# Kernel tuning notes

Measured on AMD Instinct MI355X. Metric: run time of the kernel, lower is better.

Reference implementation:

```python
import jax, jax.numpy as jnp
import numpy as np

NTS = ["User", "Group", "Computer", "Resource", "AIAgent"]
NCNT = [60000, 20000, 40000, 40000, 10000]
FEAT = [22, 6, 14, 5, 9]
# (src_nt_idx, dst_nt_idx) for the 7 active relations:
# User-MemberOf->Group, Group-MemberOf->Group, User-AdminTo->Computer,
# User-ActuallyAccessed->Resource, Computer-LSASSAccessible->Computer,
# AIAgent-AgentCanAccess->Resource, User-GenericAll->User
REL = [(0, 1), (1, 1), (0, 2), (0, 3), (2, 2), (4, 3), (0, 0)]
H, NH, L = 128, 4, 3
HD = H // NH
R = len(REL)
E = 40000


def _forward(xs, Wins, b_in, Wq, Wk, Wv, Wmsg, bmsg, rel_imp, Wo, bo, ln_g, ln_b,
             Wr1, br1, Wr2, br2, We1, be1, We2, be2, edge_index, edge_weight, theta):
    elu = jax.nn.elu
    # input projections + ELU
    h = [elu(x @ W + b_in[i]) for i, (x, W) in enumerate(zip(xs, Wins))]
    # differentiable control suppression: higher theta -> lower edge weight
    ew = edge_weight * (1.0 - jax.nn.sigmoid(theta))[:, None]  # [R, E]
    scale = HD ** -0.5
    for l in range(L):
        agg = [[] for _ in NTS]
        imps = [[] for _ in NTS]
        for r, (si, di) in enumerate(REL):
            src, dst = edge_index[r, 0], edge_index[r, 1]
            nd = h[di].shape[0]
            q = (h[di][dst] @ Wq[l, r]).reshape(-1, NH, HD)
            k = (h[si][src] @ Wk[l, r]).reshape(-1, NH, HD)
            v = (h[si][src] @ Wv[l, r]).reshape(-1, NH, HD)
            s = (q * k).sum(-1) * scale * ew[r][:, None]          # [E, NH]
            m = jax.ops.segment_max(s, dst, num_segments=nd)       # per-dst max
            ex = jnp.exp(s - m[dst])
            z = jax.ops.segment_sum(ex, dst, num_segments=nd)
            p = ex / (z[dst] + 1e-10)                              # neighborhood softmax
            msg = (v * p[..., None]).reshape(-1, H) @ Wmsg[l, r] + bmsg[l, r]
            rw = jax.nn.sigmoid(rel_imp[l, r])
            agg[di].append(jax.ops.segment_sum(msg * rw, dst, num_segments=nd))
            imps[di].append(rw)
        nh = []
        for i in range(len(NTS)):
            if agg[i]:
                w = jax.nn.softmax(jax.lax.stop_gradient(jnp.stack(imps[i])))
                comb = jnp.einsum('r,rnh->nh', w, jnp.stack(agg[i]))
                y = h[i] + comb @ Wo[l, i] + bo[l, i]
                mu = y.mean(-1, keepdims=True)
                var = ((y - mu) ** 2).mean(-1, keepdims=True)
                nh.append((y - mu) / jnp.sqrt(var + 1e-5) * ln_g[l, i] + ln_b[l, i])
            else:
                nh.append(h[i])
        h = [elu(y) for y in nh]
    risks = tuple(jax.nn.sigmoid(elu(hi @ Wr1 + br1) @ Wr2 + br2) for hi in h)
    eps = []
    for r, (si, di) in enumerate(REL):
        comb = jnp.concatenate([h[si][edge_index[r, 0]], h[di][edge_index[r, 1]]], -1)
        eps.append(jax.nn.sigmoid(elu(comb @ We1 + be1) @ We2 + be2))
    return risks + tuple(eps)


def setup_inputs() -> dict:
    key = jax.random.key(0)
    ks = iter(jax.random.split(key, 64))
    d = {}
    for nt, n, f in zip(NTS, NCNT, FEAT):
        d["x_" + nt] = jax.random.normal(next(ks), (n, f), jnp.float32)
    ei = []
    for si, di in REL:
        src = jax.random.randint(next(ks), (E,), 0, NCNT[si])
        dst = jax.random.randint(next(ks), (E,), 0, NCNT[di])
        ei.append(jnp.stack([src, dst]))
    d["edge_index"] = jnp.stack(ei).astype(jnp.int32)
    d["edge_weight"] = jax.random.uniform(next(ks), (R, E), jnp.float32)
    d["theta"] = jax.random.normal(next(ks), (R,), jnp.float32)

    def lin(k, i, o):
        return jax.random.normal(k, (i, o), jnp.float32) / float(np.sqrt(i))

    for nt, f in zip(NTS, FEAT):
        d["Win_" + nt] = lin(next(ks), f, H)
    d["b_in"] = jnp.zeros((len(NTS), H), jnp.float32)
    for nm in ["Wq", "Wk", "Wv", "Wmsg"]:
        d[nm] = jax.random.normal(next(ks), (L, R, H, H), jnp.float32) / float(np.sqrt(H))
    d["bmsg"] = jnp.zeros((L, R, H), jnp.float32)
    d["rel_imp"] = jnp.ones((L, R), jnp.float32)
    d["Wo"] = jax.random.normal(next(ks), (L, len(NTS), H, H), jnp.float32) / float(np.sqrt(H))
    d["bo"] = jnp.zeros((L, len(NTS), H), jnp.float32)
    d["ln_g"] = jnp.ones((L, len(NTS), H), jnp.float32)
    d["ln_b"] = jnp.zeros((L, len(NTS), H), jnp.float32)
    d["Wr1"] = lin(next(ks), H, H // 2)
    d["br1"] = jnp.zeros((H // 2,), jnp.float32)
    d["Wr2"] = lin(next(ks), H // 2, 1)
    d["br2"] = jnp.zeros((1,), jnp.float32)
    d["We1"] = lin(next(ks), 2 * H, H)
    d["be1"] = jnp.zeros((H,), jnp.float32)
    d["We2"] = lin(next(ks), H, 1)
    d["be2"] = jnp.zeros((1,), jnp.float32)
    return d


def reference(x_User, x_Group, x_Computer, x_Resource, x_AIAgent,
              edge_index, edge_weight, theta,
              Win_User, Win_Group, Win_Computer, Win_Resource, Win_AIAgent, b_in,
              Wq, Wk, Wv, Wmsg, bmsg, rel_imp, Wo, bo, ln_g, ln_b,
              Wr1, br1, Wr2, br2, We1, be1, We2, be2):
    xs = [x_User, x_Group, x_Computer, x_Resource, x_AIAgent]
    Wins = [Win_User, Win_Group, Win_Computer, Win_Resource, Win_AIAgent]
    return _forward(xs, Wins, b_in, Wq, Wk, Wv, Wmsg, bmsg, rel_imp, Wo, bo,
                    ln_g, ln_b, Wr1, br1, Wr2, br2, We1, be1, We2, be2,
                    edge_index, edge_weight, theta)
```

## Files before the change

### kernel.cpp

```cpp
#include <hip/hip_runtime.h>

#define CDIV(a,b) (((a)+(b)-1)/(b))
#define EE 40000
#define TOTROWS 170000
#define NDOFF 60001
#define NCHK 59
#define G_PCAT 2657

typedef unsigned short ushort_t;
typedef short bf16x8 __attribute__((ext_vector_type(8)));
typedef float f32x4 __attribute__((ext_vector_type(4)));

__device__ __forceinline__ float eluf(float x) { return x > 0.f ? x : expf(x) - 1.f; }
__device__ __forceinline__ float sigf(float x) { return 1.f / (1.f + expf(-x)); }
__device__ __forceinline__ float b2f(ushort_t u) { return __uint_as_float(((unsigned)u) << 16); }
__device__ __forceinline__ ushort_t f2b(float f) {
  unsigned x = __float_as_uint(f);
  x += 0x7FFFu + ((x >> 16) & 1u);
  return (ushort_t)(x >> 16);
}
__device__ __forceinline__ unsigned pk2(float lo, float hi) {
  return (unsigned)f2b(lo) | ((unsigned)f2b(hi) << 16);
}
__device__ __forceinline__ float2 b2f2(unsigned u) {
  return make_float2(__uint_as_float(u << 16), __uint_as_float(u & 0xFFFF0000u));
}

__constant__ const int NDD_C[7] = {20000, 20000, 40000, 40000, 40000, 40000, 60000};

__device__ __forceinline__ void stage_B128(char* Bs, int tid, const ushort_t* Bt) {
#pragma unroll
  for (int i = 0; i < 8; i++) {
    int u = tid + i * 256;
    int nrow = u >> 4;
    uint4 w = *(const uint4*)(Bt + (size_t)u * 8);
    *(uint4*)(Bs + ((u * 16) ^ ((nrow & 7) << 4))) = w;
  }
}

__device__ __forceinline__ void stage_A_bf16(char* As, int tid, const ushort_t* Ab, int base, int n) {
#pragma unroll
  for (int i = 0; i < 4; i++) {
    int u = tid + i * 256;
    int row = u >> 4;
    int grow = base + row;
    uint4 v = make_uint4(0, 0, 0, 0);
    if (grow < n) v = *(const uint4*)&Ab[(size_t)grow * 128 + (u & 15) * 8];
    *(uint4*)(As + ((u * 16) ^ ((row & 7) << 4))) = v;
  }
}

template<int NF>
__device__ __forceinline__ void mfma_core(const char* As, const char* Bs, int lane, int wcol,
                                          f32x4 (&acc)[4][NF]) {
  int i16 = lane & 15, seg = lane >> 4;
#pragma unroll
  for (int s = 0; s < 4; s++) {
    bf16x8 a[4], b[NF];
#pragma unroll
    for (int m = 0; m < 4; m++) {
      int row = m * 16 + i16;
      a[m] = *(const bf16x8*)(As + ((row * 256 + s * 64 + seg * 16) ^ ((row & 7) << 4)));
    }
#pragma unroll
    for (int nn = 0; nn < NF; nn++) {
      int nr = wcol + nn * 16 + i16;
      b[nn] = *(const bf16x8*)(Bs + ((nr * 256 + s * 64 + seg * 16) ^ ((nr & 7) << 4)));
    }
#pragma unroll
    for (int m = 0; m < 4; m++)
#pragma unroll
      for (int nn = 0; nn < NF; nn++)
        acc[m][nn] = __builtin_amdgcn_mfma_f32_16x16x32_bf16(a[m], b[nn], acc[m][nn], 0, 0, 0);
  }
}

__global__ void prep_scalars(const float* __restrict__ theta, const float* __restrict__ rel_imp,
                             float* __restrict__ scal) {
  int t = threadIdx.x;
  if (t < 7) scal[t] = 1.f - sigf(theta[t]);
  if (t < 21) {
    const int partner[7] = {1, 0, 4, 5, 2, 3, -1};
    int l = t / 7, r = t % 7;
    float rw = sigf(rel_imp[t]);
    float w;
    if (partner[r] < 0) w = 1.f;
    else {
      float rwp = sigf(rel_imp[l * 7 + partner[r]]);
      float e0 = expf(rw), e1 = expf(rwp);
      w = e0 / (e0 + e1);
    }
    scal[8 + t] = w * rw;
  }
}

__global__ __launch_bounds__(256) void transpose_weights(
    const float* __restrict__ Wq, const float* __restrict__ Wk, const float* __restrict__ Wv,
    const float* __restrict__ Wmsg, const float* __restrict__ Wo, const float* __restrict__ We1,
    ushort_t* __restrict__ Wt) {
  int mat = blockIdx.x;
  const float* src;
  if (mat < 21)      src = Wq   + (size_t)mat * 16384;
  else if (mat < 42) src = Wk   + (size_t)(mat - 21) * 16384;
  else if (mat < 63) src = Wv   + (size_t)(mat - 42) * 16384;
  else if (mat < 84) src = Wmsg + (size_t)(mat - 63) * 16384;
  else if (mat < 99) src = Wo   + (size_t)(mat - 84) * 16384;
  else               src = We1  + (size_t)(mat - 99) * 16384;
  __shared__ ushort_t lds[16384];
  int t = threadIdx.x;
  for (int i = 0; i < 64; i++) {
    int u = t + i * 256;
    int k = u >> 7;
    int byte = (u * 2) ^ ((k & 15) << 2);
    *(ushort_t*)((char*)lds + byte) = f2b(src[u]);
  }
  __syncthreads();
  ushort_t* dst = Wt + (size_t)mat * 16384;
  for (int i = 0; i < 64; i++) {
    int u = t + i * 256;
    int n = u >> 7, k = u & 127;
    int byte = ((k * 128 + n) * 2) ^ ((k & 15) << 2);
    dst[u] = *(ushort_t*)((char*)lds + byte);
  }
}

__global__ void transpose_wr1(const float* __restrict__ Wr1, ushort_t* __restrict__ Wt101) {
  int u = blockIdx.x * 256 + threadIdx.x;
  int n = u >> 7, k = u & 127;
  Wt101[u] = f2b(Wr1[k * 64 + n]);
}

template<int F>
__device__ __forceinline__ void inproj_compute(const float* xs, const float* Ws, const float* b2,
                                               ushort_t* hptr, int base, int n, int tid) {
  int cp = tid & 63, rg = tid >> 6;
  float wc0[F], wc1[F];
#pragma unroll
  for (int f = 0; f < F; f++) {
    wc0[f] = Ws[f * 128 + cp * 2];
    wc1[f] = Ws[f * 128 + cp * 2 + 1];
  }
  float bb0 = b2[cp * 2], bb1 = b2[cp * 2 + 1];
  for (int i = 0; i < 16; i++) {
    int row = rg * 16 + i, grow = base + row;
    if (grow >= n) break;
    float a0 = bb0, a1 = bb1;
#pragma unroll
    for (int f = 0; f < F; f++) {
      float xv = xs[row * F + f];
      a0 = fmaf(xv, wc0[f], a0);
      a1 = fmaf(xv, wc1[f], a1);
    }
    *(unsigned*)&hptr[(size_t)grow * 128 + cp * 2] = pk2(eluf(a0), eluf(a1));
  }
}

__global__ __launch_bounds__(256) void in_proj_all(
    const float* __restrict__ x0, const float* __restrict__ x1, const float* __restrict__ x2,
    const float* __restrict__ x3, const float* __restrict__ x4,
    const float* __restrict__ W0, const float* __restrict__ W1, const float* __restrict__ W2,
    const float* __restrict__ W3, const float* __restrict__ W4,
    const float* __restrict__ b_in, ushort_t* __restrict__ h) {
  __shared__ float xs[64 * 22];
  __shared__ float Ws[22 * 128];
  int bb = blockIdx.x, tid = threadIdx.x;
  int ti, lb;
  if (bb < 938)       { ti = 0; lb = bb; }
  else if (bb < 1251) { ti = 1; lb = bb - 938; }
  else if (bb < 1876) { ti = 2; lb = bb - 1251; }
  else if (bb < 2501) { ti = 3; lb = bb - 1876; }
  else                { ti = 4; lb = bb - 2501; }
  const int ROFF_[5] = {0, 60000, 80000, 120000, 160000};
  const int NCNT_[5] = {60000, 20000, 40000, 40000, 10000};
  const int FEAT_[5] = {22, 6, 14, 5, 9};
  const float* xp = (ti == 0) ? x0 : (ti == 1) ? x1 : (ti == 2) ? x2 : (ti == 3) ? x3 : x4;
  const float* Wp = (ti == 0) ? W0 : (ti == 1) ? W1 : (ti == 2) ? W2 : (ti == 3) ? W3 : W4;
  int F = FEAT_[ti], n = NCNT_[ti], base = lb * 64;
  for (int u = tid; u < F * 128; u += 256) Ws[u] = Wp[u];
  for (int u = tid; u < 64 * F; u += 256) {
    int row = u / F, f = u - row * F, grow = base + row;
    xs[u] = (grow < n) ? xp[(size_t)grow * F + f] : 0.f;
  }
  __syncthreads();
  ushort_t* hptr = h + (size_t)ROFF_[ti] * 128;
  const float* b2 = b_in + ti * 128;
  switch (ti) {
    case 0: inproj_compute<22>(xs, Ws, b2, hptr, base, n, tid); break;
    case 1: inproj_compute<6>(xs, Ws, b2, hptr, base, n, tid); break;
    case 2: inproj_compute<14>(xs, Ws, b2, hptr, base, n, tid); break;
    case 3: inproj_compute<5>(xs, Ws, b2, hptr, base, n, tid); break;
    default: inproj_compute<9>(xs, Ws, b2, hptr, base, n, tid); break;
  }
}

__global__ void csr_clear(int* __restrict__ counts) {
  int idx = blockIdx.x * 256 + threadIdx.x;
  if (idx < 7 * NDOFF) counts[idx] = 0;
}

__global__ void csr_hist(const int* __restrict__ ei, int* __restrict__ counts) {
  int idx = blockIdx.x * 256 + threadIdx.x;
  if (idx >= 7 * EE) return;
  int r = idx / EE, e = idx - r * EE;
  int d = ei[(size_t)r * 2 * EE + EE + e];
  atomicAdd(&counts[r * NDOFF + d], 1);
}

__global__ __launch_bounds__(256) void csr_chunk(const int* __restrict__ counts, int* __restrict__ chunkSums) {
  int bb = blockIdx.x;
  int r = bb / NCHK, c = bb - r * NCHK;
  int ndd = NDD_C[r];
  int t = threadIdx.x;
  int v = 0;
#pragma unroll
  for (int j = 0; j < 4; j++) {
    int idx = c * 1024 + t + j * 256;
    if (idx < ndd) v += counts[r * NDOFF + idx];
  }
#pragma unroll
  for (int mm = 32; mm; mm >>= 1) v += __shfl_xor(v, mm);
  __shared__ int ws_[4];
  if ((t & 63) == 0) ws_[t >> 6] = v;
  __syncthreads();
  if (t == 0) chunkSums[bb] = ws_[0] + ws_[1] + ws_[2] + ws_[3];
}

__global__ void csr_chunkscan(const int* __restrict__ chunkSums, int* __restrict__ chunkOffs) {
  int r = threadIdx.x;
  if (r >= 7) return;
  int run = 0;
  for (int c = 0; c < NCHK; c++) {
    chunkOffs[r * NCHK + c] = run;
    run += chunkSums[r * NCHK + c];
  }
}

__global__ __launch_bounds__(1024) void csr_scan_final(
    const int* __restrict__ counts, const int* __restrict__ chunkOffs,
    int* __restrict__ offs, int* __restrict__ cursor) {
  int bb = blockIdx.x;
  int r = bb / NCHK, c = bb - r * NCHK;
  int ndd = NDD_C[r];
  int t = threadIdx.x;
  int idx = c * 1024 + t;
  int v = (idx < ndd) ? counts[r * NDOFF + idx] : 0;
  __shared__ int sc[1024];
  sc[t] = v;
  __syncthreads();
  for (int s = 1; s < 1024; s <<= 1) {
    int add = (t >= s) ? sc[t - s] : 0;
    __syncthreads();
    sc[t] += add;
    __syncthreads();
  }
  if (idx < ndd) {
    int excl = chunkOffs[r * NCHK + c] + sc[t] - v;
    offs[r * NDOFF + idx] = excl;
    cursor[r * NDOFF + idx] = excl;
  }
  if (t == 0 && c == 0) offs[r * NDOFF + ndd] = EE;
}

__global__ void csr_scatter(const int* __restrict__ ei, const float* __restrict__ ew,
                            int* __restrict__ cursor, int* __restrict__ src_csr,
                            int* __restrict__ dst_csr, int* __restrict__ eid_csr,
                            float* __restrict__ ew_csr) {
  int idx = blockIdx.x * 256 + threadIdx.x;
  if (idx >= 7 * EE) return;
  int r = idx / EE, e = idx - r * EE;
  int d = ei[(size_t)r * 2 * EE + EE + e];
  int s = ei[(size_t)r * 2 * EE + e];
  int slot = atomicAdd(&cursor[r * NDOFF + d], 1);
  src_csr[r * EE + slot] = s;
  dst_csr[r * EE + slot] = d;
  eid_csr[r * EE + slot] = e;
  ew_csr[r * EE + slot] = ew[(size_t)r * EE + e];
}

template<int MODE>
__global__ __launch_bounds__(256) void msg_qkv(
    const ushort_t* __restrict__ Sb, const ushort_t* __restrict__ WtM,
    ushort_t* __restrict__ combDst, int nmsg,
    const float* __restrict__ coefp, const float* __restrict__ deg, const float* __restrict__ bvec,
    int gmsg,
    const ushort_t* __restrict__ hd, const ushort_t* __restrict__ hs,
    const ushort_t* __restrict__ WtQ, const ushort_t* __restrict__ WtK, const ushort_t* __restrict__ WtV,
    ushort_t* __restrict__ Qb, ushort_t* __restrict__ Kb, ushort_t* __restrict__ Vb,
    int ndd, int nds) {
  __shared__ char sm[16384 + 32768];
  char* As = sm;
  char* Bs = sm + 16384;
  int tid = threadIdx.x;
  int lane = tid & 63, wv = tid >> 6;
  int i16 = lane & 15, seg = lane >> 4;
  int bb = blockIdx.x;

  if (bb < gmsg) {
    int base = bb * 64;
    stage_B128(Bs, tid, WtM);
    stage_A_bf16(As, tid, Sb, base, nmsg);
    __syncthreads();
    f32x4 acc[4][2] = {};
    mfma_core<2>(As, Bs, lane, wv * 32, acc);
    float coef = *coefp;
#pragma unroll
    for (int m = 0; m < 4; m++)
#pragma unroll
      for (int i = 0; i < 4; i++) {
        int grow = base + m * 16 + seg * 4 + i;
        if (grow >= nmsg) continue;
        float dg = deg[grow];
#pragma unroll
        for (int nn = 0; nn < 2; nn++) {
          int col = wv * 32 + nn * 16 + i16;
          ushort_t* cp = &combDst[(size_t)grow * 128 + col];
          float mv = coef * (acc[m][nn][i] + dg * bvec[col]);
          if (MODE == 1) mv += b2f(*cp);
          *cp = f2b(mv);
        }
      }
    return;
  }
  bb -= gmsg;
  int nqb = (ndd + 63) >> 6;
  if (bb < nqb) {
    int base = bb * 64;
    stage_B128(Bs, tid, WtQ);
    stage_A_bf16(As, tid, hd, base, ndd);
    __syncthreads();
    f32x4 acc[4][2] = {};
    mfma_core<2>(As, Bs, lane, wv * 32, acc);
#pragma unroll
    for (int m = 0; m < 4; m++)
#pragma unroll
      for (int i = 0; i < 4; i++) {
        int grow = base + m * 16 + seg * 4 + i;
        if (grow >= ndd) continue;
#pragma unroll
        for (int nn = 0; nn < 2; nn++) {
          int col = wv * 32 + nn * 16 + i16;
          Qb[(size_t)grow * 128 + col] = f2b(acc[m][nn][i]);
        }
      }
  } else {
    int base = (bb - nqb) * 64;
    stage_A_bf16(As, tid, hs, base, nds);
    stage_B128(Bs, tid, WtK);
    __syncthreads();
    {
      f32x4 acc[4][2] = {};
      mfma_core<2>(As, Bs, lane, wv * 32, acc);
#pragma unroll
      for (int m = 0; m < 4; m++)
#pragma unroll
        for (int i = 0; i < 4; i++) {
          int grow = base + m * 16 + seg * 4 + i;
          if (grow >= nds) continue;
#pragma unroll
          for (int nn = 0; nn < 2; nn++) {
            int col = wv * 32 + nn * 16 + i16;
            Kb[(size_t)grow * 128 + col] = f2b(acc[m][nn][i]);
          }
        }
    }
    __syncthreads();
    stage_B128(Bs, tid, WtV);
    __syncthreads();
    {
      f32x4 acc[4][2] = {};
      mfma_core<2>(As, Bs, lane, wv * 32, acc);
#pragma unroll
      for (int m = 0; m < 4; m++)
#pragma unroll
        for (int i = 0; i < 4; i++) {
          int grow = base + m * 16 + seg * 4 + i;
          if (grow >= nds) continue;
#pragma unroll
          for (int nn = 0; nn < 2; nn++) {
            int col = wv * 32 + nn * 16 + i16;
            Vb[(size_t)grow * 128 + col] = f2b(acc[m][nn][i]);
          }
        }
    }
  }
}

__global__ __launch_bounds__(512) void attn_agg(
    const ushort_t* __restrict__ Qb, const ushort_t* __restrict__ Kb, const ushort_t* __restrict__ Vb,
    const int* __restrict__ offs, const int* __restrict__ src_csr, const float* __restrict__ ew_csr,
    const float* __restrict__ ews, ushort_t* __restrict__ Sb, float* __restrict__ degb, int ndd) {
  int node = blockIdx.x * 8 + (threadIdx.x >> 6);
  if (node >= ndd) return;
  int lane = threadIdx.x & 63;
  int beg = offs[node], end = offs[node + 1];
  if (end == beg) {
    Sb[(size_t)node * 128 + lane] = 0;
    Sb[(size_t)node * 128 + 64 + lane] = 0;
    if (lane == 0) degb[node] = 0.f;
    return;
  }
  float escale = ews[0] * 0.17677669529663687f;
  float q0 = b2f(Qb[(size_t)node * 128 + lane]);
  float q1 = b2f(Qb[(size_t)node * 128 + 64 + lane]);
  float m0 = -3.0e38f, m1 = -3.0e38f, z0 = 0.f, z1 = 0.f, a0 = 0.f, a1 = 0.f;
  for (int p = beg; p < end; p++) {
    int s = src_csr[p];
    float wgt = ew_csr[p] * escale;
    float k0 = b2f(Kb[(size_t)s * 128 + lane]);
    float k1 = b2f(Kb[(size_t)s * 128 + 64 + lane]);
    float p0 = q0 * k0, p1 = q1 * k1;
#pragma unroll
    for (int mm = 16; mm; mm >>= 1) {
      p0 += __shfl_xor(p0, mm);
      p1 += __shfl_xor(p1, mm);
    }
    float s0 = p0 * wgt, s1 = p1 * wgt;
    float nm0 = fmaxf(m0, s0), nm1 = fmaxf(m1, s1);
    float r0 = expf(m0 - nm0), r1 = expf(m1 - nm1);
    float e0 = expf(s0 - nm0), e1 = expf(s1 - nm1);
    float v0 = b2f(Vb[(size_t)s * 128 + lane]);
    float v1 = b2f(Vb[(size_t)s * 128 + 64 + lane]);
    z0 = z0 * r0 + e0; a0 = a0 * r0 + e0 * v0; m0 = nm0;
    z1 = z1 * r1 + e1; a1 = a1 * r1 + e1 * v1; m1 = nm1;
  }
  Sb[(size_t)node * 128 + lane]      = f2b(a0 / (z0 + 1e-10f));
  Sb[(size_t)node * 128 + 64 + lane] = f2b(a1 / (z1 + 1e-10f));
  if (lane == 0) degb[node] = (float)(end - beg);
}

#define WO_C1 938
#define WO_C2 1251
#define WO_C3 1876
#define WO_C4 2501
#define WO_TOTAL 2814
__global__ __launch_bounds__(256) void wo_ln_all(
    ushort_t* __restrict__ h, const ushort_t* __restrict__ comb, const ushort_t* __restrict__ Wt,
    const float* __restrict__ bo, const float* __restrict__ lng, const float* __restrict__ lnb, int l) {
  int bb = blockIdx.x;
  int tid = threadIdx.x;
  if (bb >= WO_C4) {
    int idx16 = (bb - WO_C4) * 256 + tid;
    if (idx16 >= 80000) return;
    ushort_t* p = h + (size_t)160000 * 128 + (size_t)idx16 * 16;
    uint4 v0 = *(uint4*)p, v1 = *(uint4*)(p + 8);
    unsigned* u0 = (unsigned*)&v0;
    unsigned* u1 = (unsigned*)&v1;
#pragma unroll
    for (int i = 0; i < 4; i++) {
      float2 a = b2f2(u0[i]); u0[i] = pk2(eluf(a.x), eluf(a.y));
      float2 b = b2f2(u1[i]); u1[i] = pk2(eluf(b.x), eluf(b.y));
    }
    *(uint4*)p = v0; *(uint4*)(p + 8) = v1;
    return;
  }
  int ti, lb;
  if (bb < WO_C1)      { ti = 0; lb = bb; }
  else if (bb < WO_C2) { ti = 1; lb = bb - WO_C1; }
  else if (bb < WO_C3) { ti = 2; lb = bb - WO_C2; }
  else                 { ti = 3; lb = bb - WO_C3; }
  const int ROFF_[4] = {0, 60000, 80000, 120000};
  const int NCNT4_[4] = {60000, 20000, 40000, 40000};
  int n = NCNT4_[ti];
  int base = lb * 64;
  int li = l * 5 + ti;
  const ushort_t* A = comb + (size_t)ROFF_[ti] * 128;
  ushort_t* C1 = h + (size_t)ROFF_[ti] * 128;
  const ushort_t* Bt = Wt + (size_t)(84 + li) * 16384;
  const float* bvec = bo + (size_t)li * 128;
  const float* g = lng + (size_t)li * 128;
  const float* b = lnb + (size_t)li * 128;

  __shared__ char sm[16384 + 32768];
  char* As = sm;
  char* Bs = sm + 16384;
  stage_B128(Bs, tid, Bt);
  stage_A_bf16(As, tid, A, base, n);
  __syncthreads();
  int lane = tid & 63, wv = tid >> 6;
  int i16 = lane & 15, seg = lane >> 4;

  f32x4 acc[8] = {};
#pragma unroll
  for (int s = 0; s < 4; s++) {
    int arow = wv * 16 + i16;
    bf16x8 a = *(const bf16x8*)(As + ((arow * 256 + s * 64 + seg * 16) ^ ((arow & 7) << 4)));
#pragma unroll
    for (int nn = 0; nn < 8; nn++) {
      int nr = nn * 16 + i16;
      bf16x8 bfr = *(const bf16x8*)(Bs + ((nr * 256 + s * 64 + seg * 16) ^ ((nr & 7) << 4)));
      acc[nn] = __builtin_amdgcn_mfma_f32_16x16x32_bf16(a, bfr, acc[nn], 0, 0, 0);
    }
  }

  float gv[8], bv[8], bov[8];
#pragma unroll
  for (int nn = 0; nn < 8; nn++) {
    int col = nn * 16 + i16;
    gv[nn] = g[col]; bv[nn] = b[col]; bov[nn] = bvec[col];
  }
#pragma unroll
  for (int i = 0; i < 4; i++) {
    int grow = base + wv * 16 + seg * 4 + i;
    if (grow >= n) continue;
    float y[8];
    float s1 = 0.f;
#pragma unroll
    for (int nn = 0; nn < 8; nn++) {
      int col = nn * 16 + i16;
      float yv = acc[nn][i] + b2f(C1[(size_t)grow * 128 + col]) + bov[nn];
      y[nn] = yv; s1 += yv;
    }
#pragma unroll
    for (int mm = 8; mm; mm >>= 1) s1 += __shfl_xor(s1, mm);
    float mu = s1 * (1.f / 128.f);
    float s2 = 0.f;
#pragma unroll
    for (int nn = 0; nn < 8; nn++) { float d = y[nn] - mu; s2 += d * d; }
#pragma unroll
    for (int mm = 8; mm; mm >>= 1) s2 += __shfl_xor(s2, mm);
    float rs = rsqrtf(s2 * (1.f / 128.f) + 1e-5f);
#pragma unroll
    for (int nn = 0; nn < 8; nn++) {
      int col = nn * 16 + i16;
      C1[(size_t)grow * 128 + col] = f2b(eluf((y[nn] - mu) * rs * gv[nn] + bv[nn]));
    }
  }
}

__global__ __launch_bounds__(256) void pcat_risk(
    const ushort_t* __restrict__ Hh, const ushort_t* __restrict__ BtP1, const ushort_t* __restrict__ BtP2,
    ushort_t* __restrict__ Pcat, const ushort_t* __restrict__ Wt101,
    const float* __restrict__ br1, const float* __restrict__ Wr2, const float* __restrict__ br2,
    float* __restrict__ out) {
  __shared__ char sm[16384 + 32768];
  char* As = sm;
  char* Bs = sm + 16384;
  int tid = threadIdx.x;
  int lane = tid & 63, wv = tid >> 6;
  int i16 = lane & 15, seg = lane >> 4;
  int bb = blockIdx.x;
  if (bb < G_PCAT) {
    int base = bb * 64;
    stage_A_bf16(As, tid, Hh, base, TOTROWS);
    stage_B128(Bs, tid, BtP1);
    __syncthreads();
    {
      f32x4 acc[4][2] = {};
      mfma_core<2>(As, Bs, lane, wv * 32, acc);
#pragma unroll
      for (int m = 0; m < 4; m++)
#pragma unroll
        for (int i = 0; i < 4; i++) {
          int grow = base + m * 16 + seg * 4 + i;
          if (grow >= TOTROWS) continue;
#pragma unroll
          for (int nn = 0; nn < 2; nn++) {
            int col = wv * 32 + nn * 16 + i16;
            Pcat[(size_t)grow * 256 + col] = f2b(acc[m][nn][i]);
          }
        }
    }
    __syncthreads();
    stage_B128(Bs, tid, BtP2);
    __syncthreads();
    {
      f32x4 acc[4][2] = {};
      mfma_core<2>(As, Bs, lane, wv * 32, acc);
#pragma unroll
      for (int m = 0; m < 4; m++)
#pragma unroll
        for (int i = 0; i < 4; i++) {
          int grow = base + m * 16 + seg * 4 + i;
          if (grow >= TOTROWS) continue;
#pragma unroll
          for (int nn = 0; nn < 2; nn++) {
            int col = 128 + wv * 32 + nn * 16 + i16;
            Pcat[(size_t)grow * 256 + col] = f2b(acc[m][nn][i]);
          }
        }
    }
  } else {
    int base = (bb - G_PCAT) * 64;
#pragma unroll
    for (int i = 0; i < 4; i++) {
      int u = tid + i * 256;
      int nrow = u >> 4;
      uint4 w = *(const uint4*)(Wt101 + (size_t)u * 8);
      *(uint4*)(Bs + ((u * 16) ^ ((nrow & 7) << 4))) = w;
    }
    stage_A_bf16(As, tid, Hh, base, TOTROWS);
    __syncthreads();
    f32x4 acc[4][1] = {};
    mfma_core<1>(As, Bs, lane, wv * 16, acc);
    __syncthreads();
    float* Hs = (float*)sm;
#pragma unroll
    for (int m = 0; m < 4; m++)
#pragma unroll
      for (int i = 0; i < 4; i++) {
        int rl = m * 16 + seg * 4 + i;
        int col = wv * 16 + i16;
        Hs[rl * 68 + col] = eluf(acc[m][0][i] + br1[col]);
      }
    __syncthreads();
    float wr2r = Wr2[lane];
    for (int rr = 0; rr < 16; rr++) {
      int rl = wv * 16 + rr;
      int grow = base + rl;
      float v = Hs[rl * 68 + lane] * wr2r;
#pragma unroll
      for (int mm = 32; mm; mm >>= 1) v += __shfl_xor(v, mm);
      if (lane == 0 && grow < TOTROWS) out[grow] = sigf(v + br2[0]);
    }
  }
}

__global__ __launch_bounds__(256) void edge_combine_all(
    const ushort_t* __restrict__ Pcat,
    const int* __restrict__ src_csr, const int* __restrict__ dst_csr, const int* __restrict__ eid_csr,
    const float* __restrict__ be1, const float* __restrict__ We2,
    const float* __restrict__ be2, float* __restrict__ out) {
  const int RSI_[7] = {0, 1, 0, 0, 2, 4, 0};
  const int RDI_[7] = {1, 1, 2, 3, 2, 3, 0};
  const int ROFF_[5] = {0, 60000, 80000, 120000, 160000};
  int bb = blockIdx.x;
  int r = bb / 10000;
  int lane = threadIdx.x & 63;
  int p = (bb % 10000) * 4 + (threadIdx.x >> 6);
  int s = src_csr[r * EE + p];
  int d = dst_csr[r * EE + p];
  int eo = eid_csr[r * EE + p];
  const unsigned* p1 = (const unsigned*)(Pcat + ((size_t)(ROFF_[RSI_[r]] + s)) * 256);
  const unsigned* p2 = (const unsigned*)(Pcat + ((size_t)(ROFF_[RDI_[r]] + d)) * 256 + 128);
  float2 a = b2f2(p1[lane]);
  float2 b = b2f2(p2[lane]);
  float2 be = *(const float2*)&be1[lane * 2];
  float2 w2 = *(const float2*)&We2[lane * 2];
  float h0 = eluf(a.x + b.x + be.x);
  float h1 = eluf(a.y + b.y + be.y);
  float v = h0 * w2.x + h1 * w2.y;
#pragma unroll
  for (int mm = 32; mm; mm >>= 1) v += __shfl_xor(v, mm);
  if (lane == 0) out[TOTROWS + (size_t)r * EE + eo] = sigf(v + be2[0]);
}

extern "C" void kernel_launch(void* const* d_in, const int* in_sizes, int n_in,
                              void* d_out, int out_size, void* d_ws, size_t ws_size,
                              hipStream_t stream) {
  (void)in_sizes; (void)n_in; (void)out_size;
  static const int NCNT_[5] = {60000, 20000, 40000, 40000, 10000};
  static const int RSI[7] = {0, 1, 0, 0, 2, 4, 0};
  static const int RDI[7] = {1, 1, 2, 3, 2, 3, 0};
  static const int RFIRST[7] = {1, 0, 1, 1, 0, 0, 1};
  static const int ROFF[5] = {0, 60000, 80000, 120000, 160000};

  const float* x[5];    for (int i = 0; i < 5; i++) x[i] = (const float*)d_in[i];
  const int*   ei     = (const int*)d_in[5];
  const float* ew     = (const float*)d_in[6];
  const float* theta  = (const float*)d_in[7];
  const float* Win[5]; for (int i = 0; i < 5; i++) Win[i] = (const float*)d_in[8 + i];
  const float* b_in   = (const float*)d_in[13];
  const float* Wq     = (const float*)d_in[14];
  const float* Wk     = (const float*)d_in[15];
  const float* Wv     = (const float*)d_in[16];
  const float* Wmsg   = (const float*)d_in[17];
  const float* bmsg   = (const float*)d_in[18];
  const float* relimp = (const float*)d_in[19];
  const float* Wo     = (const float*)d_in[20];
  const float* bo     = (const float*)d_in[21];
  const float* lng    = (const float*)d_in[22];
  const float* lnb    = (const float*)d_in[23];
  const float* Wr1    = (const float*)d_in[24];
  const float* br1    = (const float*)d_in[25];
  const float* Wr2    = (const float*)d_in[26];
  const float* br2    = (const float*)d_in[27];
  const float* We1    = (const float*)d_in[28];
  const float* be1    = (const float*)d_in[29];
  const float* We2    = (const float*)d_in[30];
  const float* be2    = (const float*)d_in[31];
  float* out = (float*)d_out;

  char* ws = (char*)d_ws;
  size_t off = 0;
  auto alloc = [&](size_t bytes) -> void* {
    void* p = (void*)(ws + off);
    off = (off + bytes + 255) & ~(size_t)255;
    return p;
  };
  ushort_t* h    = (ushort_t*)alloc((size_t)TOTROWS * 128 * 2);
  ushort_t* comb = (ushort_t*)alloc((size_t)TOTROWS * 128 * 2);
  ushort_t* Qb   = (ushort_t*)alloc((size_t)60000 * 128 * 2);
  ushort_t* Kb   = (ushort_t*)alloc((size_t)60000 * 128 * 2);
  ushort_t* Vb   = (ushort_t*)alloc((size_t)60000 * 128 * 2);
  ushort_t* Sb   = (ushort_t*)alloc((size_t)60000 * 128 * 2);
  float* degb = (float*)alloc((size_t)60000 * 4);
  ushort_t* Wt = (ushort_t*)alloc((size_t)102 * 16384 * 2);
  int* counts  = (int*)alloc((size_t)7 * NDOFF * 4);
  int* cursor  = (int*)alloc((size_t)7 * NDOFF * 4);
  int* offsb   = (int*)alloc((size_t)7 * NDOFF * 4);
  int* src_csr = (int*)alloc((size_t)7 * EE * 4);
  int* dst_csr = (int*)alloc((size_t)7 * EE * 4);
  int* eid_csr = (int*)alloc((size_t)7 * EE * 4);
  float* ew_csr = (float*)alloc((size_t)7 * EE * 4);
  int* chunkS  = (int*)alloc((size_t)7 * NCHK * 4);
  int* chunkO  = (int*)alloc((size_t)7 * NCHK * 4);
  float* scal = (float*)alloc(256);
  if (off > ws_size) return;
  ushort_t* Pcat = comb;

  prep_scalars<<<1, 64, 0, stream>>>(theta, relimp, scal);
  transpose_weights<<<101, 256, 0, stream>>>(Wq, Wk, Wv, Wmsg, Wo, We1, Wt);
  transpose_wr1<<<32, 256, 0, stream>>>(Wr1, Wt + (size_t)101 * 16384);

  in_proj_all<<<2658, 256, 0, stream>>>(
      x[0], x[1], x[2], x[3], x[4], Win[0], Win[1], Win[2], Win[3], Win[4], b_in, h);

  csr_clear<<<CDIV(7 * NDOFF, 256), 256, 0, stream>>>(counts);
  csr_hist<<<CDIV(7 * EE, 256), 256, 0, stream>>>(ei, counts);
  csr_chunk<<<7 * NCHK, 256, 0, stream>>>(counts, chunkS);
  csr_chunkscan<<<1, 64, 0, stream>>>(chunkS, chunkO);
  csr_scan_final<<<7 * NCHK, 1024, 0, stream>>>(counts, chunkO, offsb, cursor);
  csr_scatter<<<CDIV(7 * EE, 256), 256, 0, stream>>>(ei, ew, cursor, src_csr, dst_csr, eid_csr, ew_csr);

  for (int l = 0; l < 3; l++) {
    for (int r = 0; r < 7; r++) {
      int si = RSI[r], di = RDI[r];
      int nds = NCNT_[si], ndd = NCNT_[di];
      ushort_t* hs = h + (size_t)ROFF[si] * 128;
      ushort_t* hd = h + (size_t)ROFF[di] * 128;
      int lr = l * 7 + r;
      const ushort_t* WtQ = Wt + (size_t)lr * 16384;
      const ushort_t* WtK = Wt + (size_t)(21 + lr) * 16384;
      const ushort_t* WtV = Wt + (size_t)(42 + lr) * 16384;
      int gq = CDIV(ndd, 64), gkv = CDIV(nds, 64);

      if (r == 0) {
        msg_qkv<4><<<gq + gkv, 256, 0, stream>>>(
            nullptr, nullptr, nullptr, 0, scal, scal, scal, 0,
            hd, hs, WtQ, WtK, WtV, Qb, Kb, Vb, ndd, nds);
      } else {
        int pr = r - 1, plr = l * 7 + pr;
        int nmsg = NCNT_[RDI[pr]];
        int gm = CDIV(nmsg, 64);
        ushort_t* pdst = comb + (size_t)ROFF[RDI[pr]] * 128;
        const ushort_t* WtMp = Wt + (size_t)(63 + plr) * 16384;
        if (RFIRST[pr])
          msg_qkv<4><<<gm + gq + gkv, 256, 0, stream>>>(
              Sb, WtMp, pdst, nmsg, scal + 8 + plr, degb, bmsg + (size_t)plr * 128, gm,
              hd, hs, WtQ, WtK, WtV, Qb, Kb, Vb, ndd, nds);
        else
          msg_qkv<1><<<gm + gq + gkv, 256, 0, stream>>>(
              Sb, WtMp, pdst, nmsg, scal + 8 + plr, degb, bmsg + (size_t)plr * 128, gm,
              hd, hs, WtQ, WtK, WtV, Qb, Kb, Vb, ndd, nds);
      }
      attn_agg<<<CDIV(ndd, 8), 512, 0, stream>>>(
          Qb, Kb, Vb, offsb + (size_t)r * NDOFF, src_csr + (size_t)r * EE,
          ew_csr + (size_t)r * EE, scal + r, Sb, degb, ndd);
    }
    {
      int plr = l * 7 + 6;
      int nmsg = NCNT_[RDI[6]];
      int gm = CDIV(nmsg, 64);
      msg_qkv<4><<<gm, 256, 0, stream>>>(
          Sb, Wt + (size_t)(63 + plr) * 16384, comb + (size_t)ROFF[RDI[6]] * 128, nmsg,
          scal + 8 + plr, degb, bmsg + (size_t)plr * 128, gm,
          nullptr, nullptr, nullptr, nullptr, nullptr, nullptr, nullptr, nullptr, 0, 0);
    }
    wo_ln_all<<<WO_TOTAL, 256, 0, stream>>>(h, comb, Wt, bo, lng, lnb, l);
  }

  pcat_risk<<<2 * G_PCAT, 256, 0, stream>>>(
      h, Wt + (size_t)99 * 16384, Wt + (size_t)100 * 16384, Pcat,
      Wt + (size_t)101 * 16384, br1, Wr2, br2, out);

  edge_combine_all<<<7 * CDIV(EE, 4), 256, 0, stream>>>(
      Pcat, src_csr, dst_csr, eid_csr, be1, We2, be2, out);
}
```

Baseline: 1.378 ms.

## Read weight B-fragments straight from global memory instead of staging them in LDS

Every MFMA GEMM kernel (msg_qkv, the Wo/LayerNorm kernel, pcat_risk) now loads its weight-matrix B fragments directly from global memory, which should mostly hit cache. This replaces the 32 KB shared-memory staging step. Shared memory per block drops from 48 KB to 16 KB (about 33 KB in pcat_risk), which should allow more resident blocks, and several __syncthreads barriers go away. The trade-off is that each wave re-reads the weights from global/L2 with less coalesced 16-byte loads, instead of reading swizzled data from LDS.

```diff
diff --git a/kernel.cpp b/kernel.cpp
--- a/kernel.cpp
+++ b/kernel.cpp
@@ -28,16 +28,6 @@
 
 __constant__ const int NDD_C[7] = {20000, 20000, 40000, 40000, 40000, 40000, 60000};
 
-__device__ __forceinline__ void stage_B128(char* Bs, int tid, const ushort_t* Bt) {
-#pragma unroll
-  for (int i = 0; i < 8; i++) {
-    int u = tid + i * 256;
-    int nrow = u >> 4;
-    uint4 w = *(const uint4*)(Bt + (size_t)u * 8);
-    *(uint4*)(Bs + ((u * 16) ^ ((nrow & 7) << 4))) = w;
-  }
-}
-
 __device__ __forceinline__ void stage_A_bf16(char* As, int tid, const ushort_t* Ab, int base, int n) {
 #pragma unroll
   for (int i = 0; i < 4; i++) {
@@ -51,8 +41,8 @@
 }
 
 template<int NF>
-__device__ __forceinline__ void mfma_core(const char* As, const char* Bs, int lane, int wcol,
-                                          f32x4 (&acc)[4][NF]) {
+__device__ __forceinline__ void mfma_g(const char* As, const ushort_t* __restrict__ Bt,
+                                       int lane, int wcol, f32x4 (&acc)[4][NF]) {
   int i16 = lane & 15, seg = lane >> 4;
 #pragma unroll
   for (int s = 0; s < 4; s++) {
@@ -65,7 +55,7 @@
 #pragma unroll
     for (int nn = 0; nn < NF; nn++) {
       int nr = wcol + nn * 16 + i16;
-      b[nn] = *(const bf16x8*)(Bs + ((nr * 256 + s * 64 + seg * 16) ^ ((nr & 7) << 4)));
+      b[nn] = *(const bf16x8*)(Bt + (size_t)nr * 128 + s * 32 + seg * 8);
     }
 #pragma unroll
     for (int m = 0; m < 4; m++)
@@ -287,9 +277,7 @@
     const ushort_t* __restrict__ WtQ, const ushort_t* __restrict__ WtK, const ushort_t* __restrict__ WtV,
     ushort_t* __restrict__ Qb, ushort_t* __restrict__ Kb, ushort_t* __restrict__ Vb,
     int ndd, int nds) {
-  __shared__ char sm[16384 + 32768];
-  char* As = sm;
-  char* Bs = sm + 16384;
+  __shared__ char As[16384];
   int tid = threadIdx.x;
   int lane = tid & 63, wv = tid >> 6;
   int i16 = lane & 15, seg = lane >> 4;
@@ -297,11 +285,10 @@
 
   if (bb < gmsg) {
     int base = bb * 64;
-    stage_B128(Bs, tid, WtM);
     stage_A_bf16(As, tid, Sb, base, nmsg);
     __syncthreads();
     f32x4 acc[4][2] = {};
-    mfma_core<2>(As, Bs, lane, wv * 32, acc);
+    mfma_g<2>(As, WtM, lane, wv * 32, acc);
     float coef = *coefp;
 #pragma unroll
     for (int m = 0; m < 4; m++)
@@ -325,11 +312,10 @@
   int nqb = (ndd + 63) >> 6;
   if (bb < nqb) {
     int base = bb * 64;
-    stage_B128(Bs, tid, WtQ);
     stage_A_bf16(As, tid, hd, base, ndd);
     __syncthreads();
     f32x4 acc[4][2] = {};
-    mfma_core<2>(As, Bs, lane, wv * 32, acc);
+    mfma_g<2>(As, WtQ, lane, wv * 32, acc);
 #pragma unroll
     for (int m = 0; m < 4; m++)
 #pragma unroll
@@ -345,11 +331,10 @@
   } else {
     int base = (bb - nqb) * 64;
     stage_A_bf16(As, tid, hs, base, nds);
-    stage_B128(Bs, tid, WtK);
     __syncthreads();
     {
       f32x4 acc[4][2] = {};
-      mfma_core<2>(As, Bs, lane, wv * 32, acc);
+      mfma_g<2>(As, WtK, lane, wv * 32, acc);
 #pragma unroll
       for (int m = 0; m < 4; m++)
 #pragma unroll
@@ -363,12 +348,9 @@
           }
         }
     }
-    __syncthreads();
-    stage_B128(Bs, tid, WtV);
-    __syncthreads();
     {
       f32x4 acc[4][2] = {};
-      mfma_core<2>(As, Bs, lane, wv * 32, acc);
+      mfma_g<2>(As, WtV, lane, wv * 32, acc);
 #pragma unroll
       for (int m = 0; m < 4; m++)
 #pragma unroll
@@ -470,10 +452,7 @@
   const float* g = lng + (size_t)li * 128;
   const float* b = lnb + (size_t)li * 128;
 
-  __shared__ char sm[16384 + 32768];
-  char* As = sm;
-  char* Bs = sm + 16384;
-  stage_B128(Bs, tid, Bt);
+  __shared__ char As[16384];
   stage_A_bf16(As, tid, A, base, n);
   __syncthreads();
   int lane = tid & 63, wv = tid >> 6;
@@ -487,7 +466,7 @@
 #pragma unroll
     for (int nn = 0; nn < 8; nn++) {
       int nr = nn * 16 + i16;
-      bf16x8 bfr = *(const bf16x8*)(Bs + ((nr * 256 + s * 64 + seg * 16) ^ ((nr & 7) << 4)));
+      bf16x8 bfr = *(const bf16x8*)(Bt + (size_t)nr * 128 + s * 32 + seg * 8);
       acc[nn] = __builtin_amdgcn_mfma_f32_16x16x32_bf16(a, bfr, acc[nn], 0, 0, 0);
     }
   }
@@ -532,9 +511,8 @@
     ushort_t* __restrict__ Pcat, const ushort_t* __restrict__ Wt101,
     const float* __restrict__ br1, const float* __restrict__ Wr2, const float* __restrict__ br2,
     float* __restrict__ out) {
-  __shared__ char sm[16384 + 32768];
+  __shared__ char sm[16384 + 17408];
   char* As = sm;
-  char* Bs = sm + 16384;
   int tid = threadIdx.x;
   int lane = tid & 63, wv = tid >> 6;
   int i16 = lane & 15, seg = lane >> 4;
@@ -542,11 +520,12 @@
   if (bb < G_PCAT) {
     int base = bb * 64;
     stage_A_bf16(As, tid, Hh, base, TOTROWS);
-    stage_B128(Bs, tid, BtP1);
     __syncthreads();
-    {
+#pragma unroll
+    for (int half = 0; half < 2; half++) {
+      const ushort_t* Bt = half ? BtP2 : BtP1;
       f32x4 acc[4][2] = {};
-      mfma_core<2>(As, Bs, lane, wv * 32, acc);
+      mfma_g<2>(As, Bt, lane, wv * 32, acc);
 #pragma unroll
       for (int m = 0; m < 4; m++)
 #pragma unroll
@@ -555,45 +534,18 @@
           if (grow >= TOTROWS) continue;
 #pragma unroll
           for (int nn = 0; nn < 2; nn++) {
-            int col = wv * 32 + nn * 16 + i16;
+            int col = half * 128 + wv * 32 + nn * 16 + i16;
             Pcat[(size_t)grow * 256 + col] = f2b(acc[m][nn][i]);
           }
         }
     }
-    __syncthreads();
-    stage_B128(Bs, tid, BtP2);
-    __syncthreads();
-    {
-      f32x4 acc[4][2] = {};
-      mfma_core<2>(As, Bs, lane, wv * 32, acc);
-#pragma unroll
-      for (int m = 0; m < 4; m++)
-#pragma unroll
-        for (int i = 0; i < 4; i++) {
-          int grow = base + m * 16 + seg * 4 + i;
-          if (grow >= TOTROWS) continue;
-#pragma unroll
-          for (int nn = 0; nn < 2; nn++) {
-            int col = 128 + wv * 32 + nn * 16 + i16;
-            Pcat[(size_t)grow * 256 + col] = f2b(acc[m][nn][i]);
-          }
-        }
-    }
   } else {
     int base = (bb - G_PCAT) * 64;
-#pragma unroll
-    for (int i = 0; i < 4; i++) {
-      int u = tid + i * 256;
-      int nrow = u >> 4;
-      uint4 w = *(const uint4*)(Wt101 + (size_t)u * 8);
-      *(uint4*)(Bs + ((u * 16) ^ ((nrow & 7) << 4))) = w;
-    }
+    float* Hs = (float*)(sm + 16384);
     stage_A_bf16(As, tid, Hh, base, TOTROWS);
     __syncthreads();
     f32x4 acc[4][1] = {};
-    mfma_core<1>(As, Bs, lane, wv * 16, acc);
-    __syncthreads();
-    float* Hs = (float*)sm;
+    mfma_g<1>(As, Wt101, lane, wv * 16, acc);
 #pragma unroll
     for (int m = 0; m < 4; m++)
 #pragma unroll
```

Result: slower. 1.497 ms (+8.6%).
